# Kernel optimization log

Hardware: AMD Instinct MI355X
Metric: run time of the kernel (lower is better)

## Reference

```python
import jax, jax.numpy as jnp
import numpy as np

SIGMA = 1.0


def setup_inputs() -> dict:
    key = jax.random.key(0)
    z = jax.random.normal(key, (8192, 256), dtype=jnp.float32)
    return {"z": z}


def reference(z):
    n, d = z.shape
    gamma = 1.0 / (2.0 * SIGMA ** 2)
    sq = jnp.sum(z * z, axis=-1)                      # [n]
    gram = z @ z.T                                    # [n, n]
    dist_sq = sq[:, None] + sq[None, :] - 2.0 * gram  # [n, n]
    dist_sq = jnp.maximum(dist_sq, 0.0)
    term_a = jnp.mean(jnp.exp(-gamma * dist_sq))
    denom_b = 1.0 + 2.0 * gamma * SIGMA ** 2
    coeff_b = 1.0 / denom_b ** (d / 2.0)
    term_b = coeff_b * jnp.mean(jnp.exp(-(gamma / denom_b) * sq))
    term_c = 1.0 / (1.0 + 4.0 * gamma * SIGMA ** 2) ** (d / 2.0)
    return term_a - 2.0 * term_b + term_c
```

## Files before the change

kernel.cpp:

```cpp
#include <hip/hip_runtime.h>
#include <math.h>

#define N 8192
#define D 256
#define TILE 128
#define NT (N / TILE)
#define NTILES (NT * (NT + 1) / 2)
#define BK 32
#define LSTR 40
#define NPREP (N / 4)
#define LOG2E 1.4426950408889634f

typedef float f32x4 __attribute__((ext_vector_type(4)));
typedef short s16x8 __attribute__((ext_vector_type(8)));

#define WS_PB_OFF 12288
#define WS_SQ_OFF 32768
#define WS_ZB_OFF 65536

__device__ __forceinline__ ushort f32_to_bf16_rne(float x) {
    unsigned u = __float_as_uint(x);
    return (ushort)((u + 0x7FFFu + ((u >> 16) & 1u)) >> 16);
}

__global__ __launch_bounds__(256) void prep_kernel(const float* __restrict__ z,
                                                   ushort* __restrict__ zb,
                                                   float* __restrict__ sq,
                                                   float* __restrict__ partialsB) {
    __shared__ float pb4[4];
    const int t = threadIdx.x;
    const int lane = t & 63;
    const int wave = t >> 6;
    const int row = blockIdx.x * 4 + wave;
    float4 v = ((const float4*)(z + (size_t)row * D))[lane];
    ushort4 b;
    b.x = f32_to_bf16_rne(v.x);
    b.y = f32_to_bf16_rne(v.y);
    b.z = f32_to_bf16_rne(v.z);
    b.w = f32_to_bf16_rne(v.w);
    ((ushort4*)(zb + (size_t)row * D))[lane] = b;
    float s = v.x * v.x + v.y * v.y + v.z * v.z + v.w * v.w;
    #pragma unroll
    for (int off = 32; off > 0; off >>= 1) s += __shfl_xor(s, off, 64);
    if (lane == 0) {
        sq[row] = s;
        pb4[wave] = __expf(-0.25f * s);
    }
    __syncthreads();
    if (t == 0) partialsB[blockIdx.x] = pb4[0] + pb4[1] + pb4[2] + pb4[3];
}

__global__ __launch_bounds__(256) void pair_mfma_kernel(const ushort* __restrict__ zb,
                                                        const float* __restrict__ sq,
                                                        float* __restrict__ partialsA) {
    __shared__ __align__(16) ushort As[TILE][LSTR];
    __shared__ __align__(16) ushort Bs[TILE][LSTR];
    __shared__ float red[4];

    int bi = 0, rem = blockIdx.x;
    while (rem >= NT - bi) { rem -= NT - bi; ++bi; }
    const int bj = bi + rem;
    const int i0 = bi * TILE, j0 = bj * TILE;

    const int t = threadIdx.x;
    const int lane = t & 63, wave = t >> 6;
    const int wi = wave >> 1, wj = wave & 1;
    const int col = lane & 15, q = lane >> 4;

    const int sr = t >> 1;
    const int sh = t & 1;
    const ushort* gA = zb + (size_t)(i0 + sr) * D + sh * 16;
    const ushort* gB = zb + (size_t)(j0 + sr) * D + sh * 16;

    s16x8 pa0 = *(const s16x8*)(gA);
    s16x8 pa1 = *(const s16x8*)(gA + 8);
    s16x8 pb0 = *(const s16x8*)(gB);
    s16x8 pb1 = *(const s16x8*)(gB + 8);

    f32x4 acc[4][4];
    #pragma unroll
    for (int mt = 0; mt < 4; ++mt)
        #pragma unroll
        for (int nt = 0; nt < 4; ++nt)
            acc[mt][nt] = (f32x4){0.f, 0.f, 0.f, 0.f};

    for (int kc = 0; kc < D; kc += BK) {
        __syncthreads();
        *(s16x8*)&As[sr][sh * 16]     = pa0;
        *(s16x8*)&As[sr][sh * 16 + 8] = pa1;
        *(s16x8*)&Bs[sr][sh * 16]     = pb0;
        *(s16x8*)&Bs[sr][sh * 16 + 8] = pb1;
        __syncthreads();
        if (kc + BK < D) {
            pa0 = *(const s16x8*)(gA + kc + BK);
            pa1 = *(const s16x8*)(gA + kc + BK + 8);
            pb0 = *(const s16x8*)(gB + kc + BK);
            pb1 = *(const s16x8*)(gB + kc + BK + 8);
        }
        s16x8 af[4], bf[4];
        #pragma unroll
        for (int mt = 0; mt < 4; ++mt)
            af[mt] = *(const s16x8*)&As[wi * 64 + mt * 16 + col][q * 8];
        #pragma unroll
        for (int nt = 0; nt < 4; ++nt)
            bf[nt] = *(const s16x8*)&Bs[wj * 64 + nt * 16 + col][q * 8];
        #pragma unroll
        for (int mt = 0; mt < 4; ++mt)
            #pragma unroll
            for (int nt = 0; nt < 4; ++nt)
                acc[mt][nt] = __builtin_amdgcn_mfma_f32_16x16x32_bf16(
                    af[mt], bf[nt], acc[mt][nt], 0, 0, 0);
    }

    float cj[4];
    #pragma unroll
    for (int nt = 0; nt < 4; ++nt)
        cj[nt] = -0.5f * LOG2E * sq[j0 + wj * 64 + nt * 16 + col];

    float local = 0.f;
    if (bi != bj) {
        #pragma unroll
        for (int mt = 0; mt < 4; ++mt)
            #pragma unroll
            for (int r = 0; r < 4; ++r) {
                const float ci = -0.5f * LOG2E * sq[i0 + wi * 64 + mt * 16 + q * 4 + r];
                #pragma unroll
                for (int nt = 0; nt < 4; ++nt)
                    local += exp2f(fmaf(acc[mt][nt][r], LOG2E, ci) + cj[nt]);
            }
        local *= 2.f;
    } else {
        #pragma unroll
        for (int mt = 0; mt < 4; ++mt)
            #pragma unroll
            for (int r = 0; r < 4; ++r) {
                const int li = wi * 64 + mt * 16 + q * 4 + r;
                const float ci = -0.5f * LOG2E * sq[i0 + li];
                #pragma unroll
                for (int nt = 0; nt < 4; ++nt) {
                    const int lj = wj * 64 + nt * 16 + col;
                    float arg = fminf(fmaf(acc[mt][nt][r], LOG2E, ci) + cj[nt], 0.f);
                    local += (li == lj) ? 1.0f : exp2f(arg);
                }
            }
    }

    #pragma unroll
    for (int off = 32; off > 0; off >>= 1) local += __shfl_xor(local, off, 64);
    if (lane == 0) red[wave] = local;
    __syncthreads();
    if (t == 0) partialsA[blockIdx.x] = red[0] + red[1] + red[2] + red[3];
}

__global__ __launch_bounds__(256) void final_kernel(const float* __restrict__ partialsA,
                                                    const float* __restrict__ partialsB,
                                                    float* __restrict__ out) {
    __shared__ double redA[4], redB[4];
    const int t = threadIdx.x;
    double sa = 0.0, sb = 0.0;
    for (int i = t; i < NTILES; i += 256) sa += (double)partialsA[i];
    for (int i = t; i < NPREP; i += 256) sb += (double)partialsB[i];
    #pragma unroll
    for (int off = 32; off > 0; off >>= 1) {
        sa += __shfl_xor(sa, off, 64);
        sb += __shfl_xor(sb, off, 64);
    }
    if ((t & 63) == 0) { redA[t >> 6] = sa; redB[t >> 6] = sb; }
    __syncthreads();
    if (t == 0) {
        double A = redA[0] + redA[1] + redA[2] + redA[3];
        double B = redB[0] + redB[1] + redB[2] + redB[3];
        double term_a = A / ((double)N * (double)N);
        double coeff_b = ldexp(1.0, -128);
        double term_c = 1.0;
        for (int i = 0; i < 128; ++i) term_c /= 3.0;
        out[0] = (float)(term_a - 2.0 * coeff_b * (B / (double)N) + term_c);
    }
}

extern "C" void kernel_launch(void* const* d_in, const int* in_sizes, int n_in,
                              void* d_out, int out_size, void* d_ws, size_t ws_size,
                              hipStream_t stream) {
    const float* z = (const float*)d_in[0];
    float* partialsA = (float*)d_ws;
    float* partialsB = (float*)((char*)d_ws + WS_PB_OFF);
    float* sq = (float*)((char*)d_ws + WS_SQ_OFF);
    ushort* zb = (ushort*)((char*)d_ws + WS_ZB_OFF);
    float* out = (float*)d_out;

    hipLaunchKernelGGL(prep_kernel, dim3(NPREP), dim3(256), 0, stream, z, zb, sq, partialsB);
    hipLaunchKernelGGL(pair_mfma_kernel, dim3(NTILES), dim3(256), 0, stream, zb, sq, partialsA);
    hipLaunchKernelGGL(final_kernel, dim3(1), dim3(256), 0, stream, partialsA, partialsB, out);
}
```

Measured before the change: 100.0 us.

## Load MFMA operands directly from global memory, dropping LDS staging

The GEMM main loop stops staging A/B tiles through shared memory and instead has each wave load its MFMA fragments straight from global memory into registers. Register double-buffering prefetches the next K step while the current MFMAs run. This removes the LDS writes, the LDS reads and two barriers per K step. In exchange every wave issues redundant global loads (each row fragment is fetched by two waves), relying on L1/L2 to absorb them, and register pressure goes up.

```diff
diff --git a/kernel.cpp b/kernel.cpp
--- a/kernel.cpp
+++ b/kernel.cpp
@@ -6,8 +6,6 @@
 #define TILE 128
 #define NT (N / TILE)
 #define NTILES (NT * (NT + 1) / 2)
-#define BK 32
-#define LSTR 40
 #define NPREP (N / 4)
 #define LOG2E 1.4426950408889634f
 
@@ -53,8 +51,6 @@
 __global__ __launch_bounds__(256) void pair_mfma_kernel(const ushort* __restrict__ zb,
                                                         const float* __restrict__ sq,
                                                         float* __restrict__ partialsA) {
-    __shared__ __align__(16) ushort As[TILE][LSTR];
-    __shared__ __align__(16) ushort Bs[TILE][LSTR];
     __shared__ float red[4];
 
     int bi = 0, rem = blockIdx.x;
@@ -67,15 +63,13 @@
     const int wi = wave >> 1, wj = wave & 1;
     const int col = lane & 15, q = lane >> 4;
 
-    const int sr = t >> 1;
-    const int sh = t & 1;
-    const ushort* gA = zb + (size_t)(i0 + sr) * D + sh * 16;
-    const ushort* gB = zb + (size_t)(j0 + sr) * D + sh * 16;
-
-    s16x8 pa0 = *(const s16x8*)(gA);
-    s16x8 pa1 = *(const s16x8*)(gA + 8);
-    s16x8 pb0 = *(const s16x8*)(gB);
-    s16x8 pb1 = *(const s16x8*)(gB + 8);
+    const ushort* pA[4];
+    const ushort* pB[4];
+    #pragma unroll
+    for (int x = 0; x < 4; ++x) {
+        pA[x] = zb + (size_t)(i0 + wi * 64 + x * 16 + col) * D + q * 8;
+        pB[x] = zb + (size_t)(j0 + wj * 64 + x * 16 + col) * D + q * 8;
+    }
 
     f32x4 acc[4][4];
     #pragma unroll
@@ -84,32 +78,28 @@
         for (int nt = 0; nt < 4; ++nt)
             acc[mt][nt] = (f32x4){0.f, 0.f, 0.f, 0.f};
 
-    for (int kc = 0; kc < D; kc += BK) {
-        __syncthreads();
-        *(s16x8*)&As[sr][sh * 16]     = pa0;
-        *(s16x8*)&As[sr][sh * 16 + 8] = pa1;
-        *(s16x8*)&Bs[sr][sh * 16]     = pb0;
-        *(s16x8*)&Bs[sr][sh * 16 + 8] = pb1;
-        __syncthreads();
-        if (kc + BK < D) {
-            pa0 = *(const s16x8*)(gA + kc + BK);
-            pa1 = *(const s16x8*)(gA + kc + BK + 8);
-            pb0 = *(const s16x8*)(gB + kc + BK);
-            pb1 = *(const s16x8*)(gB + kc + BK + 8);
+    s16x8 af[2][4], bf[2][4];
+    #pragma unroll
+    for (int x = 0; x < 4; ++x) {
+        af[0][x] = *(const s16x8*)(pA[x]);
+        bf[0][x] = *(const s16x8*)(pB[x]);
+    }
+    #pragma unroll
+    for (int ks = 0; ks < 8; ++ks) {
+        const int cur = ks & 1, nxt = cur ^ 1;
+        if (ks < 7) {
+            #pragma unroll
+            for (int x = 0; x < 4; ++x) {
+                af[nxt][x] = *(const s16x8*)(pA[x] + (ks + 1) * 32);
+                bf[nxt][x] = *(const s16x8*)(pB[x] + (ks + 1) * 32);
+            }
         }
-        s16x8 af[4], bf[4];
-        #pragma unroll
-        for (int mt = 0; mt < 4; ++mt)
-            af[mt] = *(const s16x8*)&As[wi * 64 + mt * 16 + col][q * 8];
-        #pragma unroll
-        for (int nt = 0; nt < 4; ++nt)
-            bf[nt] = *(const s16x8*)&Bs[wj * 64 + nt * 16 + col][q * 8];
         #pragma unroll
         for (int mt = 0; mt < 4; ++mt)
             #pragma unroll
             for (int nt = 0; nt < 4; ++nt)
                 acc[mt][nt] = __builtin_amdgcn_mfma_f32_16x16x32_bf16(
-                    af[mt], bf[nt], acc[mt][nt], 0, 0, 0);
+                    af[cur][mt], bf[cur][nt], acc[mt][nt], 0, 0, 0);
     }
 
     float cj[4];
```

Measured after the change: 139.7 us. 1.4x slower.
